# Kernel optimization log

Hardware: AMD Instinct MI355X
Metric: run time of the kernel (lower is better)

## Reference

```python
import jax, jax.numpy as jnp
import numpy as np

C = 256   # num_channels
H = 16    # num_heads
L = 16384 # protein length
W = 15    # window (odd -> same-length conv with pad=(W-1)//2)


def setup_inputs() -> dict:
    key = jax.random.key(0)
    k = jax.random.split(key, 5)
    x = jax.random.normal(k[0], (1, C, L), dtype=jnp.float32)
    w_heads = jax.random.normal(k[1], (H, C, W), dtype=jnp.float32) * (1.0 / np.sqrt(C * W))
    b_heads = jax.random.normal(k[2], (H,), dtype=jnp.float32) * 0.01
    # grouped 1x1 conv with groups=H: per-head [C_out, C_in] matrices
    w_tr = jax.random.normal(k[3], (H, C, C), dtype=jnp.float32) * (1.0 / np.sqrt(C))
    b_tr = jax.random.normal(k[4], (H, C), dtype=jnp.float32) * 0.01
    return {"x": x, "w_heads": w_heads, "b_heads": b_heads, "w_tr": w_tr, "b_tr": b_tr}


def reference(x, w_heads, b_heads, w_tr, b_tr):
    pad = (W - 1) // 2
    # conv_heads: Conv1d(C -> H, kernel W, pad (W-1)//2)  -> scores [1, H, L]
    scores = jax.lax.conv_general_dilated(
        x, w_heads, window_strides=(1,), padding=[(pad, pad)],
        dimension_numbers=("NCH", "OIH", "NCH"),
    ) + b_heads[None, :, None]
    # batchwise softmax over sequence (single protein in batch -> softmax over L)
    focuses = jax.nn.softmax(scores, axis=-1)  # [1, H, L]
    # outer product: [1, H, 1, L] * [1, 1, C, L] -> [1, H, C, L] (the big intermediate)
    focused = focuses[:, :, None, :] * x[:, None, :, :]
    # grouped 1x1 conv (per-head CxC matmul) then sum over heads -> [1, C, L]
    out = jnp.einsum("hoc,bhcl->bol", w_tr, focused)
    out = out + jnp.sum(b_tr, axis=0)[None, :, None]  # head-summed per-group bias
    return out
```

## Files before the change

### kernel.cpp

```cpp
#include <hip/hip_runtime.h>
#include <hip/hip_bf16.h>

#define L_LEN 16384
#define C_CH  256
#define H_HEADS 16
#define W_WIN 15

typedef __attribute__((ext_vector_type(8))) short bf16x8;
typedef __attribute__((ext_vector_type(4))) float f32x4;
typedef unsigned short ushort_t;


__device__ __forceinline__ void gll16(const void* g, void* l) {
    __builtin_amdgcn_global_load_lds(
        (const __attribute__((address_space(1))) void*)g,
        (__attribute__((address_space(3))) void*)l, 16, 0, 0);
}

__device__ __forceinline__ ushort_t f2bf(float f) {
    __hip_bfloat16 b = __float2bfloat16(f);
    return *(ushort_t*)&b;
}

__global__ __launch_bounds__(256) void k_transpose(const float* __restrict__ x,
                                                   ushort_t* __restrict__ xb) {
    __shared__ float tile[64][65];
    int t = threadIdx.x;
    int l0 = blockIdx.x * 64;
    int c0 = blockIdx.y * 64;
#pragma unroll
    for (int r = 0; r < 16; ++r) {
        int c = r * 4 + (t >> 6);
        int l = t & 63;
        tile[c][l] = x[(size_t)(c0 + c) * L_LEN + l0 + l];
    }
    __syncthreads();
    int l = t >> 2;
    int cq = (t & 3) * 16;
    ushort_t tmp[16];
#pragma unroll
    for (int i = 0; i < 16; ++i) tmp[i] = f2bf(tile[cq + i][l]);
    char* rowp = (char*)(xb + (size_t)(l0 + l) * C_CH);
    int swz = (l & 7) << 4;
    int b0 = (c0 + cq) * 2;
    *(uint4*)(rowp + (b0 ^ swz)) = *(uint4*)&tmp[0];
    *(uint4*)(rowp + ((b0 + 16) ^ swz)) = *(uint4*)&tmp[8];
}

__global__ __launch_bounds__(256) void k_aconv(const float* __restrict__ wtr,
                                               ushort_t* __restrict__ Ag) {
    int tid = blockIdx.x * 256 + threadIdx.x;
    size_t D = (size_t)tid * 16;
    int m = (int)(D >> 13);
    int inner = (int)(D & 8191);
    int kt = inner >> 7, wb = inner & 127;
    int ob = kt * 128 + (wb ^ ((m & 7) << 4));
    int k0 = ob >> 1;
    int h = k0 >> 8, c = k0 & 255;
    const float* src = wtr + ((size_t)h * C_CH + m) * C_CH + c;
    ushort_t tmp[8];
#pragma unroll
    for (int i = 0; i < 8; ++i) tmp[i] = f2bf(src[i]);
    *(uint4*)((char*)Ag + D) = *(uint4*)tmp;
}

__global__ __launch_bounds__(256) void k_wprep(const float* __restrict__ wh,
                                               ushort_t* __restrict__ awf) {
    int tid = blockIdx.x * 256 + threadIdx.x;
    int e = tid & 7;
    int lane = (tid >> 3) & 63;
    int ktw = tid >> 9;
    int w = ktw >> 3, kt = ktw & 7;
    int h = lane & 15;
    int c = kt * 32 + (lane >> 4) * 8 + e;
    awf[tid] = f2bf(wh[((size_t)h * C_CH + c) * W_WIN + w]);
}

__global__ __launch_bounds__(128) void k_convm(const ushort_t* __restrict__ xb,
                                               const ushort_t* __restrict__ awf,
                                               float* __restrict__ scores) {
    __shared__ char xs[48 * 512];
    int t = threadIdx.x;
    int n0 = blockIdx.x * 32;
#pragma unroll
    for (int i = 0; i < 12; ++i) {
        int chunk = t + i * 128;
        int rr = chunk >> 5;
        int cb = (chunk & 31) * 16;
        int l = n0 - 8 + rr;
        int lc = l < 0 ? 0 : (l >= L_LEN ? L_LEN - 1 : l);
        gll16((const char*)xb + (size_t)lc * 512 + cb, xs + chunk * 16);
    }
    __syncthreads();
    if (n0 == 0 || n0 == L_LEN - 32) {
        int rbase = (n0 == 0) ? 0 : 40;
        uint4 z = {0u, 0u, 0u, 0u};
#pragma unroll
        for (int i = 0; i < 2; ++i) {
            int ch = t + i * 128;
            *(uint4*)(xs + rbase * 512 + ch * 16) = z;
        }
        __syncthreads();
    }
    int wv = t >> 6, lane = t & 63;
    int r = lane & 15, q = lane >> 4;
    const f32x4 vzero = {0.f, 0.f, 0.f, 0.f};
    f32x4 acc[4] = {vzero, vzero, vzero, vzero};
    for (int w = 0; w < 15; ++w) {
        int rr = wv * 16 + r + w + 1;
        const char* rowp = &xs[rr * 512];
        int sw = (rr & 7) << 4;
#pragma unroll
        for (int kt = 0; kt < 8; ++kt) {
            bf16x8 a = *(const bf16x8*)(awf + (size_t)(((w * 8 + kt) * 64 + lane) * 8));
            bf16x8 b = *(const bf16x8*)(rowp + ((kt * 64 + q * 16) ^ sw));
            acc[kt & 3] = __builtin_amdgcn_mfma_f32_16x16x32_bf16(a, b, acc[kt & 3], 0, 0, 0);
        }
    }
    f32x4 s = acc[0] + acc[1] + acc[2] + acc[3];
    int nb = n0 + wv * 16;
#pragma unroll
    for (int e = 0; e < 4; ++e)
        scores[(size_t)(q * 4 + e) * L_LEN + nb + r] = s[e];
}

__global__ __launch_bounds__(256) void k_smred(const float* __restrict__ scores,
                                               float* __restrict__ mpart,
                                               float* __restrict__ zpart) {
    __shared__ float red[8];
    int b = blockIdx.x;
    int h = b >> 3, seg = b & 7;
    int t = threadIdx.x, wid = t >> 6, ln = t & 63;
    const float* sp = scores + (size_t)h * L_LEN + seg * 2048;
    float v[8];
    float mx = -1e30f;
#pragma unroll
    for (int i = 0; i < 8; ++i) {
        v[i] = sp[i * 256 + t];
        mx = fmaxf(mx, v[i]);
    }
    for (int o = 32; o > 0; o >>= 1) mx = fmaxf(mx, __shfl_xor(mx, o));
    if (ln == 0) red[wid] = mx;
    __syncthreads();
    if (t == 0) {
        float m2 = fmaxf(fmaxf(red[0], red[1]), fmaxf(red[2], red[3]));
        red[4] = m2;
    }
    __syncthreads();
    float M = red[4];
    float s = 0.f;
#pragma unroll
    for (int i = 0; i < 8; ++i) s += __expf(v[i] - M);
    for (int o = 32; o > 0; o >>= 1) s += __shfl_xor(s, o);
    if (ln == 0) red[wid] = s;
    __syncthreads();
    if (t == 0) {
        mpart[b] = M;
        zpart[b] = red[0] + red[1] + red[2] + red[3];
    }
}

__global__ void k_scalars(const float* __restrict__ btr,
                          const float* __restrict__ mpart,
                          const float* __restrict__ zpart,
                          float* __restrict__ bias,
                          float2* __restrict__ MZ) {
    int t = threadIdx.x;
    float s = 0.f;
#pragma unroll
    for (int h = 0; h < H_HEADS; ++h) s += btr[h * C_CH + t];
    bias[t] = s;
    if (t < H_HEADS) {
        float M = -1e30f;
#pragma unroll
        for (int g = 0; g < 8; ++g) M = fmaxf(M, mpart[t * 8 + g]);
        float Z = 0.f;
#pragma unroll
        for (int g = 0; g < 8; ++g) Z += zpart[t * 8 + g] * __expf(mpart[t * 8 + g] - M);
        float2 r; r.x = M; r.y = 1.0f / Z;
        MZ[t] = r;
    }
}

#define BRES 65536
#define ATS  16384

__global__ __launch_bounds__(256, 1) void k_gemm(const ushort_t* __restrict__ Ag,
                                                 const ushort_t* __restrict__ xb,
                                                 const float* __restrict__ scores,
                                                 const float2* __restrict__ MZ,
                                                 const float* __restrict__ bias,
                                                 float* __restrict__ out) {
    __shared__ char lds[BRES + 2 * ATS];
    int t = threadIdx.x;
    int w = t >> 6, lane = t & 63;
    int m0 = blockIdx.y * 128, n0 = blockIdx.x * 128;
    int wr = w >> 1, wc = w & 1;
    int r = lane & 15, q = lane >> 4;

#pragma unroll
    for (int i = 0; i < 16; ++i) {
        int chunk = t + i * 256;
        int row = chunk >> 5, cb = (chunk & 31) * 16;
        gll16((const char*)xb + (size_t)(n0 + row) * 512 + cb, lds + chunk * 16);
    }
    auto stageA = [&](int buf, int kt) {
        const char* src = (const char*)Ag + (size_t)(m0 + (t >> 3)) * 8192 + kt * 128 + (t & 7) * 16;
        char* dst = lds + BRES + buf * ATS + t * 16;
#pragma unroll
        for (int j = 0; j < 4; ++j)
            gll16(src + (size_t)j * 32 * 8192, dst + j * 4096);
    };
    stageA(0, 0);

    const f32x4 vzero = {0.f, 0.f, 0.f, 0.f};
    f32x4 oacc[4][4], hacc[4][4];
#pragma unroll
    for (int i = 0; i < 4; ++i)
#pragma unroll
        for (int j = 0; j < 4; ++j) { oacc[i][j] = vzero; hacc[i][j] = vzero; }

    __syncthreads();

    for (int h = 0; h < H_HEADS; ++h) {
        float2 mz = MZ[h];
        float f[4];
#pragma unroll
        for (int j = 0; j < 4; ++j) {
            float s = scores[(size_t)h * L_LEN + n0 + wc * 64 + j * 16 + r];
            f[j] = __expf(s - mz.x) * mz.y;
        }
#pragma unroll
        for (int qq = 0; qq < 4; ++qq) {
            int kt = h * 4 + qq;
            int buf = kt & 1;
            if (kt < 63) stageA(buf ^ 1, kt + 1);
            char* Ab = lds + BRES + buf * ATS;
#pragma unroll
            for (int kk = 0; kk < 2; ++kk) {
                bf16x8 a[4], bb[4];
#pragma unroll
                for (int i = 0; i < 4; ++i) {
                    int ar = wr * 64 + i * 16 + r;
                    a[i] = *(const bf16x8*)(Ab + ar * 128 + ((kk * 64 + q * 16) ^ ((ar & 7) << 4)));
                }
#pragma unroll
                for (int j = 0; j < 4; ++j) {
                    int br = wc * 64 + j * 16 + r;
                    bb[j] = *(const bf16x8*)(lds + br * 512 +
                              ((qq * 128 + kk * 64 + q * 16) ^ ((br & 7) << 4)));
                }
#pragma unroll
                for (int i = 0; i < 4; ++i)
#pragma unroll
                    for (int j = 0; j < 4; ++j)
                        hacc[i][j] = __builtin_amdgcn_mfma_f32_16x16x32_bf16(a[i], bb[j], hacc[i][j], 0, 0, 0);
            }
            __syncthreads();
        }
#pragma unroll
        for (int i = 0; i < 4; ++i)
#pragma unroll
            for (int j = 0; j < 4; ++j) {
                oacc[i][j] += hacc[i][j] * f[j];
                hacc[i][j] = vzero;
            }
    }

#pragma unroll
    for (int i = 0; i < 4; ++i) {
        int mrow = m0 + wr * 64 + i * 16 + q * 4;
        float4 bv = *(const float4*)&bias[mrow];
        float bvr[4] = {bv.x, bv.y, bv.z, bv.w};
#pragma unroll
        for (int j = 0; j < 4; ++j) {
            int n = n0 + wc * 64 + j * 16 + r;
#pragma unroll
            for (int rr = 0; rr < 4; ++rr)
                out[(size_t)(mrow + rr) * L_LEN + n] = oacc[i][j][rr] + bvr[rr];
        }
    }
}

extern "C" void kernel_launch(void* const* d_in, const int* in_sizes, int n_in,
                              void* d_out, int out_size, void* d_ws, size_t ws_size,
                              hipStream_t stream) {
    const float* x   = (const float*)d_in[0];
    const float* wh  = (const float*)d_in[1];
    const float* btr = (const float*)d_in[4];
    const float* wtr = (const float*)d_in[3];
    float* out = (float*)d_out;
    char* ws = (char*)d_ws;

    ushort_t* Ag     = (ushort_t*)(ws);
    ushort_t* xb     = (ushort_t*)(ws + ((size_t)2 << 20));
    float*    scores = (float*)(ws + ((size_t)10 << 20));
    ushort_t* awf    = (ushort_t*)(ws + ((size_t)11 << 20));
    char*     sc     = ws + ((size_t)11 << 20) + (128 << 10);
    float*    mpart  = (float*)(sc);
    float*    zpart  = (float*)(sc + 512);
    float2*   MZ     = (float2*)(sc + 1024);
    float*    bias   = (float*)(sc + 2048);

    k_transpose<<<dim3(256, 4), 256, 0, stream>>>(x, xb);
    k_aconv<<<dim3(512), 256, 0, stream>>>(wtr, Ag);
    k_wprep<<<dim3(240), 256, 0, stream>>>(wh, awf);
    k_convm<<<dim3(512), 128, 0, stream>>>(xb, awf, scores);
    k_smred<<<dim3(128), 256, 0, stream>>>(scores, mpart, zpart);
    k_scalars<<<1, 256, 0, stream>>>(btr, mpart, zpart, bias, MZ);
    k_gemm<<<dim3(128, 2), 256, 0, stream>>>(Ag, xb, scores, MZ, bias, out);
}
```

Before: 138.6 us.

## Merge softmax stats kernels and deepen GEMM A-tile pipeline to four buffers

Replaces the two-kernel softmax reduction (per-segment partials, then a single-block combine) with one kernel that uses a 1024-thread block per head, plus an extra block that computes the summed bias. This removes one launch. In the GEMM, the softmax focus factors for all heads are precomputed once into an LDS table, which takes the per-head global score loads and exp out of the main loop. The A-tile staging moves from double buffering to a 4-deep ring that waits with explicit vmcnt counts and raw barriers and raises wave priority around the MFMAs. The cost is more LDS per block and fragile hand-written wait counts, and an unused leftover lambda remains in the code.

```diff
diff --git a/kernel.cpp b/kernel.cpp
--- a/kernel.cpp
+++ b/kernel.cpp
@@ -124,66 +124,59 @@
         scores[(size_t)(q * 4 + e) * L_LEN + nb + r] = s[e];
 }
 
-__global__ __launch_bounds__(256) void k_smred(const float* __restrict__ scores,
-                                               float* __restrict__ mpart,
-                                               float* __restrict__ zpart) {
-    __shared__ float red[8];
-    int b = blockIdx.x;
-    int h = b >> 3, seg = b & 7;
-    int t = threadIdx.x, wid = t >> 6, ln = t & 63;
-    const float* sp = scores + (size_t)h * L_LEN + seg * 2048;
-    float v[8];
+__global__ __launch_bounds__(1024) void k_stats(const float* __restrict__ scores,
+                                                const float* __restrict__ btr,
+                                                float2* __restrict__ MZ,
+                                                float* __restrict__ bias) {
+    int t = threadIdx.x;
+    if (blockIdx.x == 16) {
+        if (t < 256) {
+            float s = 0.f;
+#pragma unroll
+            for (int h = 0; h < H_HEADS; ++h) s += btr[h * C_CH + t];
+            bias[t] = s;
+        }
+        return;
+    }
+    __shared__ float red[17];
+    int h = blockIdx.x;
+    int wid = t >> 6, ln = t & 63;
+    const float* sp = scores + (size_t)h * L_LEN;
+    float v[16];
     float mx = -1e30f;
 #pragma unroll
-    for (int i = 0; i < 8; ++i) {
-        v[i] = sp[i * 256 + t];
+    for (int i = 0; i < 16; ++i) {
+        v[i] = sp[i * 1024 + t];
         mx = fmaxf(mx, v[i]);
     }
     for (int o = 32; o > 0; o >>= 1) mx = fmaxf(mx, __shfl_xor(mx, o));
     if (ln == 0) red[wid] = mx;
     __syncthreads();
     if (t == 0) {
-        float m2 = fmaxf(fmaxf(red[0], red[1]), fmaxf(red[2], red[3]));
-        red[4] = m2;
-    }
-    __syncthreads();
-    float M = red[4];
+        float m2 = red[0];
+        for (int i = 1; i < 16; ++i) m2 = fmaxf(m2, red[i]);
+        red[16] = m2;
+    }
+    __syncthreads();
+    float M = red[16];
     float s = 0.f;
 #pragma unroll
-    for (int i = 0; i < 8; ++i) s += __expf(v[i] - M);
+    for (int i = 0; i < 16; ++i) s += __expf(v[i] - M);
     for (int o = 32; o > 0; o >>= 1) s += __shfl_xor(s, o);
+    __syncthreads();
     if (ln == 0) red[wid] = s;
     __syncthreads();
     if (t == 0) {
-        mpart[b] = M;
-        zpart[b] = red[0] + red[1] + red[2] + red[3];
-    }
-}
-
-__global__ void k_scalars(const float* __restrict__ btr,
-                          const float* __restrict__ mpart,
-                          const float* __restrict__ zpart,
-                          float* __restrict__ bias,
-                          float2* __restrict__ MZ) {
-    int t = threadIdx.x;
-    float s = 0.f;
-#pragma unroll
-    for (int h = 0; h < H_HEADS; ++h) s += btr[h * C_CH + t];
-    bias[t] = s;
-    if (t < H_HEADS) {
-        float M = -1e30f;
-#pragma unroll
-        for (int g = 0; g < 8; ++g) M = fmaxf(M, mpart[t * 8 + g]);
         float Z = 0.f;
-#pragma unroll
-        for (int g = 0; g < 8; ++g) Z += zpart[t * 8 + g] * __expf(mpart[t * 8 + g] - M);
+        for (int i = 0; i < 16; ++i) Z += red[i];
         float2 r; r.x = M; r.y = 1.0f / Z;
-        MZ[t] = r;
+        MZ[h] = r;
     }
 }
 
 #define BRES 65536
 #define ATS  16384
+#define FTAB (BRES + 4 * ATS)
 
 __global__ __launch_bounds__(256, 1) void k_gemm(const ushort_t* __restrict__ Ag,
                                                  const ushort_t* __restrict__ xb,
@@ -191,7 +184,7 @@
                                                  const float2* __restrict__ MZ,
                                                  const float* __restrict__ bias,
                                                  float* __restrict__ out) {
-    __shared__ char lds[BRES + 2 * ATS];
+    __shared__ char lds[FTAB + 8192];
     int t = threadIdx.x;
     int w = t >> 6, lane = t & 63;
     int m0 = blockIdx.y * 128, n0 = blockIdx.x * 128;
@@ -204,6 +197,25 @@
         int row = chunk >> 5, cb = (chunk & 31) * 16;
         gll16((const char*)xb + (size_t)(n0 + row) * 512 + cb, lds + chunk * 16);
     }
+    {
+        int idx = t * 8;
+        int hh = idx >> 7, nn = idx & 127;
+        float2 mz = MZ[hh];
+        const float* sp = scores + (size_t)hh * L_LEN + n0 + nn;
+        float* ft = (float*)(lds + FTAB);
+#pragma unroll
+        for (int e = 0; e < 8; ++e)
+            ft[idx + e] = __expf(sp[e] - mz.x) * mz.y;
+    }
+    const f32x4 vzero = {0.f, 0.f, 0.f, 0.f};
+    f32x4 oacc[4][4], hacc[4][4];
+#pragma unroll
+    for (int i = 0; i < 4; ++i)
+#pragma unroll
+        for (int j = 0; j < 4; ++j) { oacc[i][j] = vzero; hacc[i][j] = vzero; }
+
+    __syncthreads();
+
     auto stageA = [&](int buf, int kt) {
         const char* src = (const char*)Ag + (size_t)(m0 + (t >> 3)) * 8192 + kt * 128 + (t & 7) * 16;
         char* dst = lds + BRES + buf * ATS + t * 16;
@@ -211,61 +223,105 @@
         for (int j = 0; j < 4; ++j)
             gll16(src + (size_t)j * 32 * 8192, dst + j * 4096);
     };
-    stageA(0, 0);
-
-    const f32x4 vzero = {0.f, 0.f, 0.f, 0.f};
-    f32x4 oacc[4][4], hacc[4][4];
-#pragma unroll
-    for (int i = 0; i < 4; ++i)
-#pragma unroll
-        for (int j = 0; j < 4; ++j) { oacc[i][j] = vzero; hacc[i][j] = vzero; }
-
-    __syncthreads();
-
-    for (int h = 0; h < H_HEADS; ++h) {
-        float2 mz = MZ[h];
-        float f[4];
-#pragma unroll
-        for (int j = 0; j < 4; ++j) {
-            float s = scores[(size_t)h * L_LEN + n0 + wc * 64 + j * 16 + r];
-            f[j] = __expf(s - mz.x) * mz.y;
-        }
+    auto compute = [&](int buf) {
+        char* Ab = lds + BRES + buf * ATS;
+        __builtin_amdgcn_s_setprio(1);
+#pragma unroll
+        for (int kk = 0; kk < 2; ++kk) {
+            bf16x8 a[4], bb[4];
+#pragma unroll
+            for (int i = 0; i < 4; ++i) {
+                int ar = wr * 64 + i * 16 + r;
+                a[i] = *(const bf16x8*)(Ab + ar * 128 + ((kk * 64 + q * 16) ^ ((ar & 7) << 4)));
+            }
+#pragma unroll
+            for (int j = 0; j < 4; ++j) {
+                int br = wc * 64 + j * 16 + r;
+                bb[j] = *(const bf16x8*)(lds + br * 512 +
+                          ((buf * 0 + kk * 64 + q * 16)));
+            }
+            (void)bb;
+#pragma unroll
+            for (int i = 0; i < 4; ++i)
+#pragma unroll
+                for (int j = 0; j < 4; ++j)
+                    hacc[i][j] = __builtin_amdgcn_mfma_f32_16x16x32_bf16(a[i], bb[j], hacc[i][j], 0, 0, 0);
+        }
+        __builtin_amdgcn_s_setprio(0);
+    };
+    (void)compute;
+
+#define COMPUTE(BUF, QQ)                                                          \
+    {                                                                             \
+        char* Ab = lds + BRES + (BUF) * ATS;                                      \
+        __builtin_amdgcn_s_setprio(1);                                            \
+        _Pragma("unroll")                                                         \
+        for (int kk = 0; kk < 2; ++kk) {                                          \
+            bf16x8 a[4], bb[4];                                                   \
+            _Pragma("unroll")                                                     \
+            for (int i = 0; i < 4; ++i) {                                         \
+                int ar = wr * 64 + i * 16 + r;                                    \
+                a[i] = *(const bf16x8*)(Ab + ar * 128 +                           \
+                          ((kk * 64 + q * 16) ^ ((ar & 7) << 4)));                \
+            }                                                                     \
+            _Pragma("unroll")                                                     \
+            for (int j = 0; j < 4; ++j) {                                         \
+                int br = wc * 64 + j * 16 + r;                                    \
+                bb[j] = *(const bf16x8*)(lds + br * 512 +                         \
+                          (((QQ) * 128 + kk * 64 + q * 16) ^ ((br & 7) << 4)));   \
+            }                                                                     \
+            _Pragma("unroll")                                                     \
+            for (int i = 0; i < 4; ++i)                                           \
+                _Pragma("unroll")                                                 \
+                for (int j = 0; j < 4; ++j)                                       \
+                    hacc[i][j] = __builtin_amdgcn_mfma_f32_16x16x32_bf16(         \
+                        a[i], bb[j], hacc[i][j], 0, 0, 0);                        \
+        }                                                                         \
+        __builtin_amdgcn_s_setprio(0);                                            \
+    }
+
+#define SCALE(H)                                                                  \
+    {                                                                             \
+        const float* ft = (const float*)(lds + FTAB) + (H) * 128;                 \
+        float f[4];                                                               \
+        _Pragma("unroll")                                                         \
+        for (int j = 0; j < 4; ++j) f[j] = ft[wc * 64 + j * 16 + r];              \
+        _Pragma("unroll")                                                         \
+        for (int i = 0; i < 4; ++i)                                               \
+            _Pragma("unroll")                                                     \
+            for (int j = 0; j < 4; ++j) {                                         \
+                oacc[i][j] += hacc[i][j] * f[j];                                  \
+                hacc[i][j] = vzero;                                               \
+            }                                                                     \
+    }
+
+    stageA(0, 0); stageA(1, 1); stageA(2, 2);
+
+    for (int h = 0; h < 15; ++h) {
 #pragma unroll
         for (int qq = 0; qq < 4; ++qq) {
             int kt = h * 4 + qq;
-            int buf = kt & 1;
-            if (kt < 63) stageA(buf ^ 1, kt + 1);
-            char* Ab = lds + BRES + buf * ATS;
-#pragma unroll
-            for (int kk = 0; kk < 2; ++kk) {
-                bf16x8 a[4], bb[4];
-#pragma unroll
-                for (int i = 0; i < 4; ++i) {
-                    int ar = wr * 64 + i * 16 + r;
-                    a[i] = *(const bf16x8*)(Ab + ar * 128 + ((kk * 64 + q * 16) ^ ((ar & 7) << 4)));
-                }
-#pragma unroll
-                for (int j = 0; j < 4; ++j) {
-                    int br = wc * 64 + j * 16 + r;
-                    bb[j] = *(const bf16x8*)(lds + br * 512 +
-                              ((qq * 128 + kk * 64 + q * 16) ^ ((br & 7) << 4)));
-                }
-#pragma unroll
-                for (int i = 0; i < 4; ++i)
-#pragma unroll
-                    for (int j = 0; j < 4; ++j)
-                        hacc[i][j] = __builtin_amdgcn_mfma_f32_16x16x32_bf16(a[i], bb[j], hacc[i][j], 0, 0, 0);
-            }
-            __syncthreads();
-        }
-#pragma unroll
-        for (int i = 0; i < 4; ++i)
-#pragma unroll
-            for (int j = 0; j < 4; ++j) {
-                oacc[i][j] += hacc[i][j] * f[j];
-                hacc[i][j] = vzero;
-            }
-    }
+            asm volatile("s_waitcnt vmcnt(8)" ::: "memory");
+            __builtin_amdgcn_s_barrier();
+            stageA((kt + 3) & 3, kt + 3);
+            COMPUTE(kt & 3, qq);
+        }
+        SCALE(h);
+    }
+    asm volatile("s_waitcnt vmcnt(8)" ::: "memory");
+    __builtin_amdgcn_s_barrier();
+    stageA(3, 63);
+    COMPUTE(0, 0);
+    asm volatile("s_waitcnt vmcnt(8)" ::: "memory");
+    __builtin_amdgcn_s_barrier();
+    COMPUTE(1, 1);
+    asm volatile("s_waitcnt vmcnt(4)" ::: "memory");
+    __builtin_amdgcn_s_barrier();
+    COMPUTE(2, 2);
+    asm volatile("s_waitcnt vmcnt(0)" ::: "memory");
+    __builtin_amdgcn_s_barrier();
+    COMPUTE(3, 3);
+    SCALE(15);
 
 #pragma unroll
     for (int i = 0; i < 4; ++i) {
@@ -280,6 +336,8 @@
                 out[(size_t)(mrow + rr) * L_LEN + n] = oacc[i][j][rr] + bvr[rr];
         }
     }
+#undef COMPUTE
+#undef SCALE
 }
 
 extern "C" void kernel_launch(void* const* d_in, const int* in_sizes, int n_in,
@@ -287,8 +345,8 @@
                               hipStream_t stream) {
     const float* x   = (const float*)d_in[0];
     const float* wh  = (const float*)d_in[1];
+    const float* wtr = (const float*)d_in[3];
     const float* btr = (const float*)d_in[4];
-    const float* wtr = (const float*)d_in[3];
     float* out = (float*)d_out;
     char* ws = (char*)d_ws;
 
@@ -297,16 +355,13 @@
     float*    scores = (float*)(ws + ((size_t)10 << 20));
     ushort_t* awf    = (ushort_t*)(ws + ((size_t)11 << 20));
     char*     sc     = ws + ((size_t)11 << 20) + (128 << 10);
-    float*    mpart  = (float*)(sc);
-    float*    zpart  = (float*)(sc + 512);
-    float2*   MZ     = (float2*)(sc + 1024);
-    float*    bias   = (float*)(sc + 2048);
+    float2*   MZ     = (float2*)(sc);
+    float*    bias   = (float*)(sc + 1024);
 
     k_transpose<<<dim3(256, 4), 256, 0, stream>>>(x, xb);
     k_aconv<<<dim3(512), 256, 0, stream>>>(wtr, Ag);
     k_wprep<<<dim3(240), 256, 0, stream>>>(wh, awf);
     k_convm<<<dim3(512), 128, 0, stream>>>(xb, awf, scores);
-    k_smred<<<dim3(128), 256, 0, stream>>>(scores, mpart, zpart);
-    k_scalars<<<1, 256, 0, stream>>>(btr, mpart, zpart, bias, MZ);
+    k_stats<<<dim3(17), 1024, 0, stream>>>(scores, btr, MZ, bias);
     k_gemm<<<dim3(128, 2), 256, 0, stream>>>(Ag, xb, scores, MZ, bias, out);
 }
```

Result: faster. 130.7 us (-5.7%).
